# Kernel tuning notes

Hardware: AMD Instinct MI355X
Metric: run time of the kernel (lower is better)

Reference implementation:

```python
import jax, jax.numpy as jnp
import numpy as np

D = 256; NH = 8; NL = 4; NP = 4; DH = D // NH; DFFN = 1024; NQ = 900; BS = 4
SPATIAL = ((92, 92), (46, 46), (23, 23), (12, 12))  # (H, W) per level
LEVEL_START = (0, 8464, 10580, 11109)
S = sum(h * w for h, w in SPATIAL)  # 11253


def _ln(x, g, b):
    m = jnp.mean(x, -1, keepdims=True)
    v = jnp.var(x, -1, keepdims=True)
    return (x - m) / jnp.sqrt(v + 1e-5) * g + b


def setup_inputs() -> dict:
    key = jax.random.key(0)
    ks = jax.random.split(key, 24)
    p = lambda k, s: 0.02 * jax.random.normal(k, s, jnp.float32)
    return {
        "tgt": jax.random.normal(ks[0], (NQ, BS, D), jnp.float32),
        "tgt_query_pos": jax.random.normal(ks[1], (NQ, BS, D), jnp.float32),
        "tgt_reference_points": jax.random.uniform(ks[2], (NQ, BS, NL, 2), jnp.float32),
        "memory": jax.random.normal(ks[3], (S, BS, D), jnp.float32),
        "memory_spatial_shapes": jnp.array(SPATIAL, jnp.int32),
        "memory_level_start_index": jnp.array(LEVEL_START, jnp.int32),
        "in_proj_w": p(ks[4], (3 * D, D)), "in_proj_b": p(ks[5], (3 * D,)),
        "out_proj_w": p(ks[6], (D, D)), "out_proj_b": p(ks[7], (D,)),
        "off_w": p(ks[8], (NH * NL * NP * 2, D)), "off_b": p(ks[9], (NH * NL * NP * 2,)),
        "aw_w": p(ks[10], (NH * NL * NP, D)), "aw_b": p(ks[11], (NH * NL * NP,)),
        "vproj_w": p(ks[12], (D, D)), "vproj_b": p(ks[13], (D,)),
        "oproj_w": p(ks[14], (D, D)), "oproj_b": p(ks[15], (D,)),
        "ln1_g": jnp.ones((D,), jnp.float32), "ln1_b": jnp.zeros((D,), jnp.float32),
        "ln2_g": jnp.ones((D,), jnp.float32), "ln2_b": jnp.zeros((D,), jnp.float32),
        "ln3_g": jnp.ones((D,), jnp.float32), "ln3_b": jnp.zeros((D,), jnp.float32),
        "lin1_w": p(ks[16], (DFFN, D)), "lin1_b": p(ks[17], (DFFN,)),
        "lin2_w": p(ks[18], (D, DFFN)), "lin2_b": p(ks[19], (D,)),
    }


def _self_attn(q, k, v, in_w, in_b, out_w, out_b):
    # q, k, v: (nq, bs, d) -- torch nn.MultiheadAttention, eval mode
    wq, wk, wv = jnp.split(in_w, 3, axis=0)
    bq, bk, bv = jnp.split(in_b, 3)
    qp = (q @ wq.T + bq).reshape(NQ, BS, NH, DH)
    kp = (k @ wk.T + bk).reshape(NQ, BS, NH, DH)
    vp = (v @ wv.T + bv).reshape(NQ, BS, NH, DH)
    s = jnp.einsum("qbhd,kbhd->bhqk", qp, kp) / jnp.sqrt(jnp.float32(DH))
    a = jax.nn.softmax(s, axis=-1)
    o = jnp.einsum("bhqk,kbhd->qbhd", a, vp).reshape(NQ, BS, D)
    return o @ out_w.T + out_b


def _msdeform(x, ref, mem, off_w, off_b, aw_w, aw_b, vproj_w, vproj_b, oproj_w, oproj_b):
    # x: (bs, nq, d); ref: (bs, nq, nl, 2) in [0,1]; mem: (bs, S, d)
    value = (mem @ vproj_w.T + vproj_b).reshape(BS, S, NH, DH)
    off = (x @ off_w.T + off_b).reshape(BS, NQ, NH, NL, NP, 2)
    aw = jax.nn.softmax((x @ aw_w.T + aw_b).reshape(BS, NQ, NH, NL * NP), axis=-1)
    aw = aw.reshape(BS, NQ, NH, NL, NP)
    # offset normalizer = (W, H) per level
    norm = jnp.array([[w, h] for (h, w) in SPATIAL], jnp.float32)
    loc = ref[:, :, None, :, None, :] + off / norm[None, None, None, :, None, :]
    out = jnp.zeros((BS, NH, NQ, DH), x.dtype)
    for l, (H, W) in enumerate(SPATIAL):
        s0 = LEVEL_START[l]
        v = value[:, s0:s0 + H * W].transpose(0, 2, 1, 3)  # (bs, nh, H*W, dh)
        g = loc[:, :, :, l].transpose(0, 2, 1, 3, 4)       # (bs, nh, nq, np, 2)
        # grid_sample align_corners=False, padding_mode='zeros'
        px = g[..., 0] * W - 0.5
        py = g[..., 1] * H - 0.5
        x0 = jnp.floor(px).astype(jnp.int32)
        y0 = jnp.floor(py).astype(jnp.int32)
        wx = px - x0
        wy = py - y0
        samp = jnp.zeros((BS, NH, NQ, NP, DH), x.dtype)
        for dx, dy, w in ((0, 0, (1 - wx) * (1 - wy)), (1, 0, wx * (1 - wy)),
                          (0, 1, (1 - wx) * wy), (1, 1, wx * wy)):
            xi = x0 + dx
            yi = y0 + dy
            valid = ((xi >= 0) & (xi < W) & (yi >= 0) & (yi < H)).astype(x.dtype)
            idx = (jnp.clip(yi, 0, H - 1) * W + jnp.clip(xi, 0, W - 1)).reshape(BS, NH, NQ * NP)
            gat = jnp.take_along_axis(v, idx[..., None], axis=2).reshape(BS, NH, NQ, NP, DH)
            samp = samp + (w * valid)[..., None] * gat
        a = aw[:, :, :, l].transpose(0, 2, 1, 3)  # (bs, nh, nq, np)
        out = out + (samp * a[..., None]).sum(axis=3)
    out = out.transpose(0, 2, 1, 3).reshape(BS, NQ, D)
    return out @ oproj_w.T + oproj_b


def reference(tgt, tgt_query_pos, tgt_reference_points, memory,
              memory_spatial_shapes, memory_level_start_index,
              in_proj_w, in_proj_b, out_proj_w, out_proj_b,
              off_w, off_b, aw_w, aw_b, vproj_w, vproj_b, oproj_w, oproj_b,
              ln1_g, ln1_b, ln2_g, ln2_b, ln3_g, ln3_b,
              lin1_w, lin1_b, lin2_w, lin2_b):
    # module_seq = ['sa', 'ca', 'ffn']; dropout inactive (eval)
    q = tgt + tgt_query_pos
    tgt2 = _self_attn(q, q, tgt, in_proj_w, in_proj_b, out_proj_w, out_proj_b)
    tgt = _ln(tgt + tgt2, ln2_g, ln2_b)
    x = (tgt + tgt_query_pos).transpose(1, 0, 2)
    ref = tgt_reference_points.transpose(1, 0, 2, 3)
    mem = memory.transpose(1, 0, 2)
    tgt2 = _msdeform(x, ref, mem, off_w, off_b, aw_w, aw_b,
                     vproj_w, vproj_b, oproj_w, oproj_b).transpose(1, 0, 2)
    tgt = _ln(tgt + tgt2, ln1_g, ln1_b)
    ff = jax.nn.relu(tgt @ lin1_w.T + lin1_b) @ lin2_w.T + lin2_b
    return _ln(tgt + ff, ln3_g, ln3_b)
```

## Files before the change

### kernel.cpp

```cpp
#include <hip/hip_runtime.h>
#include <math.h>

#define D_MODEL 256
#define NHEAD   8
#define NLVL    4
#define NPTS    4
#define DHEAD   32
#define DFFN    1024
#define NQ      900
#define BSZ     4
#define NROW    (NQ * BSZ)
#define S_TOT   11253
#define VROWS   (S_TOT * BSZ)
#define SASCALE 0.17677669529663687f

typedef __attribute__((ext_vector_type(8))) short short8;
typedef __attribute__((ext_vector_type(4))) float f32x4;
typedef unsigned short ushort_t;

static __device__ __forceinline__ unsigned f2bf1(float f) {
    unsigned u = __float_as_uint(f);
    return (u + 0x7FFFu + ((u >> 16) & 1u)) >> 16;
}
static __device__ __forceinline__ unsigned pack2bf(float x, float y) {
// ... 17 lines not shown

__global__ __launch_bounds__(256) void cvt_weights(
    const float* __restrict__ w_in, const float* __restrict__ w_vp,
    const float* __restrict__ w_outp, const float* __restrict__ w_off,
    const float* __restrict__ w_aw, const float* __restrict__ w_op,
    const float* __restrict__ w_l1, const float* __restrict__ w_l2,
    ushort_t* __restrict__ dst)
{
    int b = blockIdx.x;
    const float* src;
    int dstoff;
    if (b < 96)       { src = w_in;   dstoff = WB_IN;   }
    else if (b < 128) { src = w_vp;   b -= 96;  dstoff = WB_VP;   }
    else if (b < 160) { src = w_outp; b -= 128; dstoff = WB_OUTP; }
    else if (b < 192) { src = w_off;  b -= 160; dstoff = WB_OFF;  }
    else if (b < 208) { src = w_aw;   b -= 192; dstoff = WB_AW;   }
    else if (b < 240) { src = w_op;   b -= 208; dstoff = WB_OP;   }
    else if (b < 368) { src = w_l1;   b -= 240; dstoff = WB_L1;   }
    else              { src = w_l2;   b -= 368; dstoff = WB_L2;   }
    int i = (b * 256 + threadIdx.x) * 8;
    float4 f0 = *(const float4*)(src + i);
    float4 f1 = *(const float4*)(src + i + 4);
    uint4 u;
    u.x = pack2bf(f0.x, f0.y); u.y = pack2bf(f0.z, f0.w);
    u.z = pack2bf(f1.x, f1.y); u.w = pack2bf(f1.z, f1.w);
    *(uint4*)(dst + dstoff + i) = u;
}

__global__ __launch_bounds__(256) void proj_fused(
    const float* __restrict__ tgt, const float* __restrict__ qpos,
    const ushort_t* __restrict__ in_wb, const float* __restrict__ in_b,
    const float* __restrict__ mem, const ushort_t* __restrict__ vp_wb,
    const float* __restrict__ vp_b,
    ushort_t* __restrict__ qkv16, ushort_t* __restrict__ value16)
{
    __shared__ ushort_t As[64 * GPAD];
    __shared__ ushort_t Ws[128 * GPAD];

    const int t    = threadIdx.x;
    const int bid  = blockIdx.x;
    const int trow = t >> 2;
    const int tk   = (t & 3) << 4;
    const int wv   = t >> 6;
    const int ln   = t & 63;
    const int L    = ln & 15;
    const int quad = ln >> 4;

    if (bid < 684) {
        const int m0 = (bid % 57) * 64;
        const int n0 = (bid / 57) * 64;
        const bool addpos = (n0 < 512);
        const float oscale = (n0 < 256) ? SASCALE : 1.f;

        f32x4 acc[4] = {{0.f,0.f,0.f,0.f},{0.f,0.f,0.f,0.f},
                        {0.f,0.f,0.f,0.f},{0.f,0.f,0.f,0.f}};

        for (int k0 = 0; k0 < 256; k0 += 64) {
            {
                int m = m0 + trow;
                float4 a0, a1, a2, a3;
                if (m < NROW) {
                    const float* ap = tgt + (size_t)m * 256 + k0 + tk;
                    a0 = *(const float4*)(ap + 0);
                    a1 = *(const float4*)(ap + 4);
                    a2 = *(const float4*)(ap + 8);
                    a3 = *(const float4*)(ap + 12);
                    if (addpos) {
                        const float* pp = qpos + (size_t)m * 256 + k0 + tk;
                        float4 p0 = *(const float4*)(pp + 0);
                        float4 p1 = *(const float4*)(pp + 4);
                        float4 p2 = *(const float4*)(pp + 8);
                        float4 p3 = *(const float4*)(pp + 12);
                        a0.x += p0.x; a0.y += p0.y; a0.z += p0.z; a0.w += p0.w;
                        a1.x += p1.x; a1.y += p1.y; a1.z += p1.z; a1.w += p1.w;
                        a2.x += p2.x; a2.y += p2.y; a2.z += p2.z; a2.w += p2.w;
                        a3.x += p3.x; a3.y += p3.y; a3.z += p3.z; a3.w += p3.w;
                    }
                } else {
                    a0 = a1 = a2 = a3 = make_float4(0.f, 0.f, 0.f, 0.f);
                }
                uint4 u0, u1;
                u0.x = pack2bf(a0.x, a0.y); u0.y = pack2bf(a0.z, a0.w);
                u0.z = pack2bf(a1.x, a1.y); u0.w = pack2bf(a1.z, a1.w);
                u1.x = pack2bf(a2.x, a2.y); u1.y = pack2bf(a2.z, a2.w);
                u1.z = pack2bf(a3.x, a3.y); u1.w = pack2bf(a3.z, a3.w);
                *(uint4*)&As[trow * GPAD + tk + 0] = u0;
                *(uint4*)&As[trow * GPAD + tk + 8] = u1;
            }
            {
                int n = n0 + trow;
                const ushort_t* wp = in_wb + (size_t)n * 256 + k0 + tk;
                *(uint4*)&Ws[trow * GPAD + tk + 0] = *(const uint4*)(wp + 0);
                *(uint4*)&Ws[trow * GPAD + tk + 8] = *(const uint4*)(wp + 8);
            }
            __syncthreads();
#pragma unroll
            for (int kh = 0; kh < 2; ++kh) {
                short8 af = *(const short8*)&As[(wv * 16 + L) * GPAD + kh * 32 + quad * 8];
#pragma unroll
                for (int cb = 0; cb < 4; ++cb) {
                    short8 bf = *(const short8*)&Ws[(cb * 16 + L) * GPAD + kh * 32 + quad * 8];
                    acc[cb] = __builtin_amdgcn_mfma_f32_16x16x32_bf16(af, bf, acc[cb], 0, 0, 0);
                }
            }
            __syncthreads();
        }
#pragma unroll
        for (int cb = 0; cb < 4; ++cb) {
            int col = n0 + cb * 16 + L;
            float bv = in_b[col];
#pragma unroll
            for (int i = 0; i < 4; ++i) {
                int m = m0 + wv * 16 + quad * 4 + i;
                if (m < NROW)
                    qkv16[(size_t)m * 768 + col] = (ushort_t)f2bf1((acc[cb][i] + bv) * oscale);
            }
        }
    } else {
        const int vb = bid - 684;
        const int m0 = (vb >> 1) * 64;
        const int nh = (vb & 1) * 128;

        f32x4 acc[8];
#pragma unroll
        for (int i = 0; i < 8; ++i) acc[i] = (f32x4){0.f, 0.f, 0.f, 0.f};

        for (int k0 = 0; k0 < 256; k0 += 64) {
            {
                int m = m0 + trow;
                float4 a0, a1, a2, a3;
                if (m < VROWS) {
                    const float* ap = mem + (size_t)m * 256 + k0 + tk;
                    a0 = *(const float4*)(ap + 0);
                    a1 = *(const float4*)(ap + 4);
                    a2 = *(const float4*)(ap + 8);
                    a3 = *(const float4*)(ap + 12);
                } else {
                    a0 = a1 = a2 = a3 = make_float4(0.f, 0.f, 0.f, 0.f);
                }
                uint4 u0, u1;
                u0.x = pack2bf(a0.x, a0.y); u0.y = pack2bf(a0.z, a0.w);
                u0.z = pack2bf(a1.x, a1.y); u0.w = pack2bf(a1.z, a1.w);
                u1.x = pack2bf(a2.x, a2.y); u1.y = pack2bf(a2.z, a2.w);
                u1.z = pack2bf(a3.x, a3.y); u1.w = pack2bf(a3.z, a3.w);
                *(uint4*)&As[trow * GPAD + tk + 0] = u0;
                *(uint4*)&As[trow * GPAD + tk + 8] = u1;
            }
#pragma unroll
            for (int wb = 0; wb < 2; ++wb) {
                int n = wb * 64 + trow;
                const ushort_t* wp = vp_wb + (size_t)(nh + n) * 256 + k0 + tk;
                *(uint4*)&Ws[n * GPAD + tk + 0] = *(const uint4*)(wp + 0);
                *(uint4*)&Ws[n * GPAD + tk + 8] = *(const uint4*)(wp + 8);
            }
            __syncthreads();
#pragma unroll
            for (int kh = 0; kh < 2; ++kh) {
                short8 af = *(const short8*)&As[(wv * 16 + L) * GPAD + kh * 32 + quad * 8];
#pragma unroll
                for (int cb = 0; cb < 8; ++cb) {
                    short8 bf = *(const short8*)&Ws[(cb * 16 + L) * GPAD + kh * 32 + quad * 8];
                    acc[cb] = __builtin_amdgcn_mfma_f32_16x16x32_bf16(af, bf, acc[cb], 0, 0, 0);
                }
            }
            __syncthreads();
        }

        ushort_t* Cs = Ws;
#pragma unroll
        for (int cb = 0; cb < 8; ++cb) {
            int col = cb * 16 + L;
            float bv = vp_b[nh + col];
#pragma unroll
            for (int i = 0; i < 4; ++i) {
                int r = wv * 16 + quad * 4 + i;
                Cs[r * 136 + col] = (ushort_t)f2bf1(acc[cb][i] + bv);
            }
        }
        __syncthreads();
        {
            int r  = t >> 2;
            int ch = (t & 3) * 32;
            int m  = m0 + r;
            if (m < VROWS) {
                const ushort_t* src = &Cs[r * 136 + ch];
                uint4* dst = (uint4*)(value16 + (size_t)m * 256 + nh + ch);
#pragma unroll
                for (int j = 0; j < 4; ++j)
                    dst[j] = *(const uint4*)(src + j * 8);
            }
        }
    }
}

__global__ __launch_bounds__(256) void sa_flash16(
    const ushort_t* __restrict__ qkv, ushort_t* __restrict__ attn_out)
{
    __shared__ ushort_t Ks[2 * 2080];
    __shared__ ushort_t Vt[2 * 2304];
    __shared__ ushort_t Ps[4 * 1152];

    const int t    = threadIdx.x;
    const int q0   = blockIdx.x * 64;
    const int b    = blockIdx.y & 3;
    const int h    = blockIdx.y >> 2;
    const int wv   = t >> 6;
    const int ln   = t & 63;
    const int L    = ln & 15;
    const int quad = ln >> 4;

    union { uint4 u; short8 s; } qu;
    qu.u = make_uint4(0u, 0u, 0u, 0u);
    {
        int q = q0 + wv * 16 + L;
        if (q < NQ)
            qu.u = *(const uint4*)(qkv + ((size_t)q * 4 + b) * 768 + h * 32 + quad * 8);
    }
    const short8 qf = qu.s;

    float mrun = -1e30f, lrun = 0.f;
    f32x4 oacc[2] = {{0.f,0.f,0.f,0.f},{0.f,0.f,0.f,0.f}};

    const int skey = t >> 2;
    const int sdg  = t & 3;

    int it = 0;
    for (int k0 = 0; k0 < NQ; k0 += 64, it ^= 1) {
        {
            int kg = k0 + skey;
            uint4 ku = make_uint4(0u,0u,0u,0u), vu = make_uint4(0u,0u,0u,0u);
            if (kg < NQ) {
                const ushort_t* base = qkv + ((size_t)kg * 4 + b) * 768 + 256 + h * 32 + sdg * 8;
                ku = *(const uint4*)base;
                vu = *(const uint4*)(base + 256);
            }
            *(uint4*)&Ks[it * 2080 + sdg * 520 + skey * 8] = ku;
            ushort_t* vp = &Vt[it * 2304 + sdg * 8 * 72 + skey];
            vp[0 * 72] = (ushort_t)(vu.x & 0xffffu);
            vp[1 * 72] = (ushort_t)(vu.x >> 16);
            vp[2 * 72] = (ushort_t)(vu.y & 0xffffu);
            vp[3 * 72] = (ushort_t)(vu.y >> 16);
            vp[4 * 72] = (ushort_t)(vu.z & 0xffffu);
            vp[5 * 72] = (ushort_t)(vu.z >> 16);
            vp[6 * 72] = (ushort_t)(vu.w & 0xffffu);
            vp[7 * 72] = (ushort_t)(vu.w >> 16);
        }
        __syncthreads();

        f32x4 sacc[4] = {{0.f,0.f,0.f,0.f},{0.f,0.f,0.f,0.f},
                         {0.f,0.f,0.f,0.f},{0.f,0.f,0.f,0.f}};
#pragma unroll
        for (int cb = 0; cb < 4; ++cb) {
            short8 kf = *(const short8*)&Ks[it * 2080 + quad * 520 + (cb * 16 + L) * 8];
            sacc[cb] = __builtin_amdgcn_mfma_f32_16x16x32_bf16(kf, qf, sacc[cb], 0, 0, 0);
        }
        if (k0 + 64 > NQ) {
#pragma unroll
            for (int cb = 0; cb < 4; ++cb)
#pragma unroll
                for (int i = 0; i < 4; ++i)
                    if (k0 + cb * 16 + quad * 4 + i >= NQ) sacc[cb][i] = -1e30f;
        }

        float ml = -1e30f;
#pragma unroll
        for (int cb = 0; cb < 4; ++cb)
#pragma unroll
            for (int i = 0; i < 4; ++i) ml = fmaxf(ml, sacc[cb][i]);
        ml = fmaxf(ml, __shfl_xor(ml, 16, 64));
        ml = fmaxf(ml, __shfl_xor(ml, 32, 64));
        float mnew  = fmaxf(mrun, ml);
        float alpha = __expf(mrun - mnew);
        float p[16];
        float rs = 0.f;
#pragma unroll
        for (int cb = 0; cb < 4; ++cb)
#pragma unroll
            for (int i = 0; i < 4; ++i) {
                float e = __expf(sacc[cb][i] - mnew);
                p[cb * 4 + i] = e;
                rs += e;
            }
        rs += __shfl_xor(rs, 16, 64);
        rs += __shfl_xor(rs, 32, 64);
        lrun = lrun * alpha + rs;
        mrun = mnew;

        {
            ushort_t* pw = &Ps[wv * 1152 + L * 72];
#pragma unroll
            for (int cb = 0; cb < 4; ++cb) {
                uint2 u;
                u.x = pack2bf(p[cb * 4 + 0], p[cb * 4 + 1]);
                u.y = pack2bf(p[cb * 4 + 2], p[cb * 4 + 3]);
                *(uint2*)&pw[cb * 16 + quad * 4] = u;
            }
        }
#pragma unroll
        for (int i = 0; i < 4; ++i) {
            float ai = __shfl(alpha, quad * 4 + i, 64);
            oacc[0][i] *= ai;
            oacc[1][i] *= ai;
        }
        __syncthreads();

#pragma unroll
        for (int ks = 0; ks < 2; ++ks) {
            short8 pf = *(const short8*)&Ps[wv * 1152 + L * 72 + ks * 32 + quad * 8];
#pragma unroll
            for (int db = 0; db < 2; ++db) {
                short8 vf = *(const short8*)&Vt[it * 2304 + (db * 16 + L) * 72 + ks * 32 + quad * 8];
                oacc[db] = __builtin_amdgcn_mfma_f32_16x16x32_bf16(pf, vf, oacc[db], 0, 0, 0);
            }
        }
    }

#pragma unroll
    for (int i = 0; i < 4; ++i) {
        float lq = __shfl(lrun, quad * 4 + i, 64);
        float li = 1.f / lq;
        int q = q0 + wv * 16 + quad * 4 + i;
        if (q < NQ) {
            ushort_t* op = attn_out + ((size_t)q * 4 + b) * 256 + h * 32 + L;
            op[0]  = (ushort_t)f2bf1(oacc[0][i] * li);
            op[16] = (ushort_t)f2bf1(oacc[1][i] * li);
        }
    }
}

__global__ __launch_bounds__(256) void gemm16_f32(
    const ushort_t* __restrict__ A, const ushort_t* __restrict__ W,
    const float* __restrict__ bias, float* __restrict__ C,
    int M, int N, int K, int ldc)
{
    __shared__ ushort_t As[64 * GPAD];
    __shared__ ushort_t Ws[64 * GPAD];

    const int t  = threadIdx.x;
    const int m0 = blockIdx.x * 64;
    const int n0 = blockIdx.y * 64;
    const int trow = t >> 2;
    const int tk   = (t & 3) << 4;
    const int wv   = t >> 6;
    const int ln   = t & 63;
    const int L    = ln & 15;
    const int quad = ln >> 4;

    f32x4 acc[4] = {{0.f,0.f,0.f,0.f},{0.f,0.f,0.f,0.f},
                    {0.f,0.f,0.f,0.f},{0.f,0.f,0.f,0.f}};

    for (int k0 = 0; k0 < K; k0 += 64) {
        {
            int m = m0 + trow;
            uint4 a0 = make_uint4(0u,0u,0u,0u), a1 = make_uint4(0u,0u,0u,0u);
            if (m < M) {
                const ushort_t* ap = A + (size_t)m * K + k0 + tk;
                a0 = *(const uint4*)ap;
                a1 = *(const uint4*)(ap + 8);
            }
            *(uint4*)&As[trow * GPAD + tk + 0] = a0;
            *(uint4*)&As[trow * GPAD + tk + 8] = a1;
        }
        {
            int n = n0 + trow;
            const ushort_t* wp = W + (size_t)n * K + k0 + tk;
            *(uint4*)&Ws[trow * GPAD + tk + 0] = *(const uint4*)(wp + 0);
            *(uint4*)&Ws[trow * GPAD + tk + 8] = *(const uint4*)(wp + 8);
        }
        __syncthreads();
#pragma unroll
        for (int kh = 0; kh < 2; ++kh) {
            short8 af = *(const short8*)&As[(wv * 16 + L) * GPAD + kh * 32 + quad * 8];
#pragma unroll
            for (int cb = 0; cb < 4; ++cb) {
                short8 bf = *(const short8*)&Ws[(cb * 16 + L) * GPAD + kh * 32 + quad * 8];
                acc[cb] = __builtin_amdgcn_mfma_f32_16x16x32_bf16(af, bf, acc[cb], 0, 0, 0);
            }
        }
        __syncthreads();
    }
#pragma unroll
    for (int cb = 0; cb < 4; ++cb) {
        int col = n0 + cb * 16 + L;
        float bv = bias[col];
#pragma unroll
        for (int i = 0; i < 4; ++i) {
            int m = m0 + wv * 16 + quad * 4 + i;
            if (m < M)
                C[(size_t)m * ldc + col] = acc[cb][i] + bv;
        }
    }
}

__global__ __launch_bounds__(256) void ln_resid16(
    const float* __restrict__ xa, const float* __restrict__ xb,
    const float* __restrict__ gam, const float* __restrict__ bet,
    float* __restrict__ out, const float* __restrict__ pos,
    ushort_t* __restrict__ out2)
{
    const int row = blockIdx.x;
    const int t = threadIdx.x;
    float x = xa[(size_t)row * D_MODEL + t] + xb[(size_t)row * D_MODEL + t];
    float s = x, s2 = x * x;
#pragma unroll
    for (int off = 32; off > 0; off >>= 1) {
        s  += __shfl_down(s, off, 64);
        s2 += __shfl_down(s2, off, 64);
    }
    __shared__ float rs[4], rs2[4];
    __shared__ float mean_s, rstd_s;
    int wid = t >> 6, lane = t & 63;
    if (lane == 0) { rs[wid] = s; rs2[wid] = s2; }
    __syncthreads();
    if (t == 0) {
        float S = rs[0] + rs[1] + rs[2] + rs[3];
        float S2 = rs2[0] + rs2[1] + rs2[2] + rs2[3];
        float mean = S * (1.f / 256.f);
        float var = S2 * (1.f / 256.f) - mean * mean;
        mean_s = mean;
        rstd_s = rsqrtf(var + 1e-5f);
    }
    __syncthreads();
    float y = (x - mean_s) * rstd_s * gam[t] + bet[t];
    out[(size_t)row * D_MODEL + t] = y;
    if (out2) {
        float o2 = y + (pos ? pos[(size_t)row * D_MODEL + t] : 0.f);
        out2[(size_t)row * D_MODEL + t] = (ushort_t)f2bf1(o2);
    }
}

__global__ __launch_bounds__(256) void offaw16(
    const ushort_t* __restrict__ A,
    const ushort_t* __restrict__ off_wb, const float* __restrict__ off_b,
    const ushort_t* __restrict__ aw_wb, const float* __restrict__ aw_b,
    float* __restrict__ off_raw, float* __restrict__ aw_raw)
{
    __shared__ ushort_t As[64 * GPAD];
    __shared__ ushort_t Ws[64 * GPAD];

    const int t  = threadIdx.x;
    const int m0 = blockIdx.x * 64;
    const int by = blockIdx.y;
    const bool isaw = (by >= 4);
    const int n0 = isaw ? (by - 4) * 64 : by * 64;
    const ushort_t* W = isaw ? aw_wb : off_wb;
    const float* bs = isaw ? aw_b : off_b;
    float* C = isaw ? aw_raw : off_raw;
    const int ldc = isaw ? 128 : 256;

    const int trow = t >> 2;
    const int tk   = (t & 3) << 4;
    const int wv   = t >> 6;
    const int ln   = t & 63;
    const int L    = ln & 15;
    const int quad = ln >> 4;

    f32x4 acc[4] = {{0.f,0.f,0.f,0.f},{0.f,0.f,0.f,0.f},
                    {0.f,0.f,0.f,0.f},{0.f,0.f,0.f,0.f}};

    for (int k0 = 0; k0 < 256; k0 += 64) {
        {
            int m = m0 + trow;
            uint4 a0 = make_uint4(0u,0u,0u,0u), a1 = make_uint4(0u,0u,0u,0u);
            if (m < NROW) {
                const ushort_t* ap = A + (size_t)m * 256 + k0 + tk;
                a0 = *(const uint4*)ap;
                a1 = *(const uint4*)(ap + 8);
            }
            *(uint4*)&As[trow * GPAD + tk + 0] = a0;
            *(uint4*)&As[trow * GPAD + tk + 8] = a1;
        }
        {
            int n = n0 + trow;
            const ushort_t* wp = W + (size_t)n * 256 + k0 + tk;
            *(uint4*)&Ws[trow * GPAD + tk + 0] = *(const uint4*)(wp + 0);
            *(uint4*)&Ws[trow * GPAD + tk + 8] = *(const uint4*)(wp + 8);
        }
        __syncthreads();
#pragma unroll
        for (int kh = 0; kh < 2; ++kh) {
            short8 af = *(const short8*)&As[(wv * 16 + L) * GPAD + kh * 32 + quad * 8];
#pragma unroll
            for (int cb = 0; cb < 4; ++cb) {
                short8 bf = *(const short8*)&Ws[(cb * 16 + L) * GPAD + kh * 32 + quad * 8];
                acc[cb] = __builtin_amdgcn_mfma_f32_16x16x32_bf16(af, bf, acc[cb], 0, 0, 0);
            }
        }
        __syncthreads();
    }
#pragma unroll
    for (int cb = 0; cb < 4; ++cb) {
        int col = n0 + cb * 16 + L;
        float bv = bs[col];
#pragma unroll
        for (int i = 0; i < 4; ++i) {
            int m = m0 + wv * 16 + quad * 4 + i;
            if (m < NROW)
                C[(size_t)m * ldc + col] = acc[cb][i] + bv;
        }
    }
}

__global__ __launch_bounds__(256) void gemm16_16(
    const ushort_t* __restrict__ A, const ushort_t* __restrict__ W,
    const float* __restrict__ bias, ushort_t* __restrict__ C,
    int M, int N, int K, int ldc, int relu)
{
    __shared__ ushort_t As[64 * GPAD];
    __shared__ ushort_t Ws[64 * GPAD];

    const int t  = threadIdx.x;
    const int m0 = blockIdx.x * 64;
    const int n0 = blockIdx.y * 64;
    const int trow = t >> 2;
    const int tk   = (t & 3) << 4;
    const int wv   = t >> 6;
    const int ln   = t & 63;
    const int L    = ln & 15;
    const int quad = ln >> 4;

    f32x4 acc[4] = {{0.f,0.f,0.f,0.f},{0.f,0.f,0.f,0.f},
                    {0.f,0.f,0.f,0.f},{0.f,0.f,0.f,0.f}};

    for (int k0 = 0; k0 < K; k0 += 64) {
        {
            int m = m0 + trow;
            uint4 a0 = make_uint4(0u,0u,0u,0u), a1 = make_uint4(0u,0u,0u,0u);
            if (m < M) {
                const ushort_t* ap = A + (size_t)m * K + k0 + tk;
                a0 = *(const uint4*)ap;
                a1 = *(const uint4*)(ap + 8);
            }
            *(uint4*)&As[trow * GPAD + tk + 0] = a0;
            *(uint4*)&As[trow * GPAD + tk + 8] = a1;
        }
        {
            int n = n0 + trow;
            const ushort_t* wp = W + (size_t)n * K + k0 + tk;
            *(uint4*)&Ws[trow * GPAD + tk + 0] = *(const uint4*)(wp + 0);
            *(uint4*)&Ws[trow * GPAD + tk + 8] = *(const uint4*)(wp + 8);
        }
        __syncthreads();
#pragma unroll
        for (int kh = 0; kh < 2; ++kh) {
            short8 af = *(const short8*)&As[(wv * 16 + L) * GPAD + kh * 32 + quad * 8];
#pragma unroll
            for (int cb = 0; cb < 4; ++cb) {
                short8 bf = *(const short8*)&Ws[(cb * 16 + L) * GPAD + kh * 32 + quad * 8];
                acc[cb] = __builtin_amdgcn_mfma_f32_16x16x32_bf16(af, bf, acc[cb], 0, 0, 0);
            }
        }
        __syncthreads();
    }
#pragma unroll
    for (int cb = 0; cb < 4; ++cb) {
        int col = n0 + cb * 16 + L;
        float bv = bias[col];
#pragma unroll
        for (int i = 0; i < 4; ++i) {
            int m = m0 + wv * 16 + quad * 4 + i;
            if (m < M) {
                float o = acc[cb][i] + bv;
                if (relu) o = fmaxf(o, 0.f);
                C[(size_t)m * ldc + col] = (ushort_t)f2bf1(o);
            }
        }
    }
}

__global__ __launch_bounds__(256) void msdeform16(
    const float* __restrict__ off_raw, const float* __restrict__ aw_raw,
    const float* __restrict__ refp, const ushort_t* __restrict__ value,
    ushort_t* __restrict__ out)
{
    const int row = blockIdx.x;
    const int b = row & 3;
    const int t = threadIdx.x;

    __shared__ float aw_s[8][17];
    __shared__ float px_s[8][16];
    __shared__ float py_s[8][16];

    const int Hs[4]  = {92, 46, 23, 12};
    const int Wd[4]  = {92, 46, 23, 12};
    const int S0_[4] = {0, 8464, 10580, 11109};

    if (t < 128) {
        int hh = t >> 4, lp = t & 15, l = lp >> 2;
        float ox = off_raw[(size_t)row * 256 + hh * 32 + lp * 2 + 0];
        float oy = off_raw[(size_t)row * 256 + hh * 32 + lp * 2 + 1];
        float rx = refp[((size_t)row * 4 + l) * 2 + 0];
// ... 37 lines not shown
            for (int dy = 0; dy < 2; ++dy) {
#pragma unroll
                for (int dx = 0; dx < 2; ++dx) {
                    int xi = x0 + dx, yi = y0 + dy;
                    float flag = (xi >= 0 && xi < W && yi >= 0 && yi < H) ? 1.f : 0.f;
                    int xc = xi < 0 ? 0 : (xi >= W ? W - 1 : xi);
                    int yc = yi < 0 ? 0 : (yi >= H ? H - 1 : yi);
                    float wgt = (dx ? wx : 1.f - wx) * (dy ? wy : 1.f - wy);
                    float gv = bf2f(vb[(size_t)(base + yc * W + xc) * 1024]);
                    sv = fmaf(wgt * flag, gv, sv);
                }
            }
            acc = fmaf(aw_s[h][lp], sv, acc);
        }
    }
    out[(size_t)row * 256 + h * 32 + d] = (ushort_t)f2bf1(acc);
}

extern "C" void kernel_launch(void* const* d_in, const int* in_sizes, int n_in,
                              void* d_out, int out_size, void* d_ws, size_t ws_size,
                              hipStream_t stream)
{
    const float* tgt    = (const float*)d_in[0];
    const float* qpos   = (const float*)d_in[1];
    const float* refp   = (const float*)d_in[2];
    const float* mem    = (const float*)d_in[3];
    const float* in_w   = (const float*)d_in[6];
    const float* in_b   = (const float*)d_in[7];
    const float* outp_w = (const float*)d_in[8];
    const float* outp_b = (const float*)d_in[9];
    const float* off_w  = (const float*)d_in[10];
    const float* off_b  = (const float*)d_in[11];
    const float* aw_w   = (const float*)d_in[12];
    const float* aw_b   = (const float*)d_in[13];
    const float* vp_w   = (const float*)d_in[14];
    const float* vp_b   = (const float*)d_in[15];
    const float* op_w   = (const float*)d_in[16];
    const float* op_b   = (const float*)d_in[17];
    const float* ln1g   = (const float*)d_in[18];
    const float* ln1b   = (const float*)d_in[19];
    const float* ln2g   = (const float*)d_in[20];
    const float* ln2b   = (const float*)d_in[21];
    const float* ln3g   = (const float*)d_in[22];
    const float* ln3b   = (const float*)d_in[23];
    const float* l1w    = (const float*)d_in[24];
    const float* l1b    = (const float*)d_in[25];
    const float* l2w    = (const float*)d_in[26];
    const float* l2b    = (const float*)d_in[27];
    float* out = (float*)d_out;
    float* ws  = (float*)d_ws;

    ushort_t* qkv16    = (ushort_t*)ws;
    ushort_t* att16    = (ushort_t*)(ws + 691200);
    float*    tmp      = ws + 921600;
    float*    tgt_a    = ws + 1843200;
    ushort_t* xca16    = (ushort_t*)(ws + 2764800);
    float*    off_raw  = ws + 2995200;
    float*    aw_raw   = ws + 3916800;
    ushort_t* att2_16  = (ushort_t*)(ws + 4377600);
    float*    tgt_b    = ws + 4608000;
    ushort_t* tgtb16   = (ushort_t*)(ws + 5529600);
    ushort_t* value16  = (ushort_t*)(ws + 5760000);
    ushort_t* hidden16 = (ushort_t*)(ws + 11521536);
    ushort_t* wb       = (ushort_t*)(ws + 13364736);

    const ushort_t* in_wb   = wb + WB_IN;
    const ushort_t* vp_wb   = wb + WB_VP;
    const ushort_t* outp_wb = wb + WB_OUTP;
    const ushort_t* off_wb  = wb + WB_OFF;
    const ushort_t* aw_wb   = wb + WB_AW;
    const ushort_t* op_wb   = wb + WB_OP;
    const ushort_t* l1_wb   = wb + WB_L1;
    const ushort_t* l2_wb   = wb + WB_L2;

    dim3 b256(256);

    hipLaunchKernelGGL(cvt_weights, dim3(496), b256, 0, stream,
                       in_w, vp_w, outp_w, off_w, aw_w, op_w, l1w, l2w, wb);
    hipLaunchKernelGGL(proj_fused, dim3(2092), b256, 0, stream,
                       tgt, qpos, in_wb, in_b, mem, vp_wb, vp_b, qkv16, value16);
    hipLaunchKernelGGL(sa_flash16, dim3(15, 32), b256, 0, stream, qkv16, att16);
    hipLaunchKernelGGL(gemm16_f32, dim3(57, 4), b256, 0, stream,
                       att16, outp_wb, outp_b, tmp, NROW, 256, 256, 256);
    hipLaunchKernelGGL(ln_resid16, dim3(3600), b256, 0, stream,
                       tgt, tmp, ln2g, ln2b, tgt_a, qpos, xca16);
    hipLaunchKernelGGL(offaw16, dim3(57, 6), b256, 0, stream,
                       xca16, off_wb, off_b, aw_wb, aw_b, off_raw, aw_raw);
    hipLaunchKernelGGL(msdeform16, dim3(3600), b256, 0, stream,
                       off_raw, aw_raw, refp, value16, att2_16);
    hipLaunchKernelGGL(gemm16_f32, dim3(57, 4), b256, 0, stream,
                       att2_16, op_wb, op_b, tmp, NROW, 256, 256, 256);
    hipLaunchKernelGGL(ln_resid16, dim3(3600), b256, 0, stream,
                       tgt_a, tmp, ln1g, ln1b, tgt_b, (const float*)nullptr, tgtb16);
    hipLaunchKernelGGL(gemm16_16, dim3(57, 16), b256, 0, stream,
                       tgtb16, l1_wb, l1b, hidden16, NROW, 1024, 256, 1024, 1);
    hipLaunchKernelGGL(gemm16_f32, dim3(57, 4), b256, 0, stream,
                       hidden16, l2_wb, l2b, tmp, NROW, 256, 1024, 256);
    hipLaunchKernelGGL(ln_resid16, dim3(3600), b256, 0, stream,
                       tgt_b, tmp, ln3g, ln3b, out, (const float*)nullptr, (ushort_t*)nullptr);
}
```

Baseline: 278.9 us.

## Fuse output GEMMs with residual LayerNorm, widen value-proj tile, prefetch K/V

Three GEMM+residual+LayerNorm pairs are merged into one gemm_ln16 kernel. Each block computes a full 64x256 row tile and reduces mean and variance in registers with shuffles, which removes the fp32 tmp round trip and three launches. The value projection now computes all 256 output columns per block, reusing each converted memory tile across both weight halves. Flash self-attention register-prefetches the next K/V tile. Only 57 blocks now cover each fused GEMM, which cuts parallelism, and the 256-row weight tile in shared memory raises per-block footprint.

```diff
diff --git a/kernel.cpp b/kernel.cpp
--- a/kernel.cpp
+++ b/kernel.cpp
@@ -93,44 +93,45 @@
         const bool addpos = (n0 < 512);
         const float oscale = (n0 < 256) ? SASCALE : 1.f;
 
+        const int  mrow = m0 + trow;
+        const bool mv   = (mrow < NROW);
+        const float* arow = tgt  + (size_t)mrow * 256 + tk;
+        const float* prow = qpos + (size_t)mrow * 256 + tk;
+        const ushort_t* wrow = in_wb + (size_t)(n0 + trow) * 256 + tk;
+
         f32x4 acc[4] = {{0.f,0.f,0.f,0.f},{0.f,0.f,0.f,0.f},
                         {0.f,0.f,0.f,0.f},{0.f,0.f,0.f,0.f}};
 
         for (int k0 = 0; k0 < 256; k0 += 64) {
-            {
-                int m = m0 + trow;
-                float4 a0, a1, a2, a3;
-                if (m < NROW) {
-                    const float* ap = tgt + (size_t)m * 256 + k0 + tk;
-                    a0 = *(const float4*)(ap + 0);
-                    a1 = *(const float4*)(ap + 4);
-                    a2 = *(const float4*)(ap + 8);
-                    a3 = *(const float4*)(ap + 12);
-                    if (addpos) {
-                        const float* pp = qpos + (size_t)m * 256 + k0 + tk;
-                        float4 p0 = *(const float4*)(pp + 0);
-                        float4 p1 = *(const float4*)(pp + 4);
-                        float4 p2 = *(const float4*)(pp + 8);
-                        float4 p3 = *(const float4*)(pp + 12);
-                        a0.x += p0.x; a0.y += p0.y; a0.z += p0.z; a0.w += p0.w;
-                        a1.x += p1.x; a1.y += p1.y; a1.z += p1.z; a1.w += p1.w;
-                        a2.x += p2.x; a2.y += p2.y; a2.z += p2.z; a2.w += p2.w;
-                        a3.x += p3.x; a3.y += p3.y; a3.z += p3.z; a3.w += p3.w;
-                    }
-                } else {
-                    a0 = a1 = a2 = a3 = make_float4(0.f, 0.f, 0.f, 0.f);
+            uint4 u0, u1;
+            if (mv) {
+                const float* ap = arow + k0;
+                float4 a0 = *(const float4*)(ap + 0);
+                float4 a1 = *(const float4*)(ap + 4);
+                float4 a2 = *(const float4*)(ap + 8);
+                float4 a3 = *(const float4*)(ap + 12);
+                if (addpos) {
+                    const float* pp = prow + k0;
+                    float4 p0 = *(const float4*)(pp + 0);
+                    float4 p1 = *(const float4*)(pp + 4);
+                    float4 p2 = *(const float4*)(pp + 8);
+                    float4 p3 = *(const float4*)(pp + 12);
+                    a0.x += p0.x; a0.y += p0.y; a0.z += p0.z; a0.w += p0.w;
+                    a1.x += p1.x; a1.y += p1.y; a1.z += p1.z; a1.w += p1.w;
+                    a2.x += p2.x; a2.y += p2.y; a2.z += p2.z; a2.w += p2.w;
+                    a3.x += p3.x; a3.y += p3.y; a3.z += p3.z; a3.w += p3.w;
                 }
-                uint4 u0, u1;
                 u0.x = pack2bf(a0.x, a0.y); u0.y = pack2bf(a0.z, a0.w);
                 u0.z = pack2bf(a1.x, a1.y); u0.w = pack2bf(a1.z, a1.w);
                 u1.x = pack2bf(a2.x, a2.y); u1.y = pack2bf(a2.z, a2.w);
                 u1.z = pack2bf(a3.x, a3.y); u1.w = pack2bf(a3.z, a3.w);
-                *(uint4*)&As[trow * GPAD + tk + 0] = u0;
-                *(uint4*)&As[trow * GPAD + tk + 8] = u1;
-            }
+            } else {
+                u0 = make_uint4(0u, 0u, 0u, 0u); u1 = u0;
+            }
+            *(uint4*)&As[trow * GPAD + tk + 0] = u0;
+            *(uint4*)&As[trow * GPAD + tk + 8] = u1;
             {
-                int n = n0 + trow;
-                const ushort_t* wp = in_wb + (size_t)n * 256 + k0 + tk;
+                const ushort_t* wp = wrow + k0;
                 *(uint4*)&Ws[trow * GPAD + tk + 0] = *(const uint4*)(wp + 0);
                 *(uint4*)&Ws[trow * GPAD + tk + 8] = *(const uint4*)(wp + 8);
             }
@@ -159,38 +160,37 @@
         }
     } else {
         const int vb = bid - 684;
-        const int m0 = (vb >> 1) * 64;
-        const int nh = (vb & 1) * 128;
-
-        f32x4 acc[8];
-#pragma unroll
-        for (int i = 0; i < 8; ++i) acc[i] = (f32x4){0.f, 0.f, 0.f, 0.f};
+        const int m0 = vb * 64;
+
+        const int  mrow = m0 + trow;
+        const bool mv   = (mrow < VROWS);
+        const float* arow = mem + (size_t)mrow * 256 + tk;
+
+        f32x4 acc[16];
+#pragma unroll
+        for (int i = 0; i < 16; ++i) acc[i] = (f32x4){0.f, 0.f, 0.f, 0.f};
 
         for (int k0 = 0; k0 < 256; k0 += 64) {
-            {
-                int m = m0 + trow;
-                float4 a0, a1, a2, a3;
-                if (m < VROWS) {
-                    const float* ap = mem + (size_t)m * 256 + k0 + tk;
-                    a0 = *(const float4*)(ap + 0);
-                    a1 = *(const float4*)(ap + 4);
-                    a2 = *(const float4*)(ap + 8);
-                    a3 = *(const float4*)(ap + 12);
-                } else {
-                    a0 = a1 = a2 = a3 = make_float4(0.f, 0.f, 0.f, 0.f);
-                }
-                uint4 u0, u1;
+            uint4 u0, u1;
+            if (mv) {
+                const float* ap = arow + k0;
+                float4 a0 = *(const float4*)(ap + 0);
+                float4 a1 = *(const float4*)(ap + 4);
+                float4 a2 = *(const float4*)(ap + 8);
+                float4 a3 = *(const float4*)(ap + 12);
                 u0.x = pack2bf(a0.x, a0.y); u0.y = pack2bf(a0.z, a0.w);
                 u0.z = pack2bf(a1.x, a1.y); u0.w = pack2bf(a1.z, a1.w);
                 u1.x = pack2bf(a2.x, a2.y); u1.y = pack2bf(a2.z, a2.w);
                 u1.z = pack2bf(a3.x, a3.y); u1.w = pack2bf(a3.z, a3.w);
-                *(uint4*)&As[trow * GPAD + tk + 0] = u0;
-                *(uint4*)&As[trow * GPAD + tk + 8] = u1;
-            }
-#pragma unroll
-            for (int wb = 0; wb < 2; ++wb) {
-                int n = wb * 64 + trow;
-                const ushort_t* wp = vp_wb + (size_t)(nh + n) * 256 + k0 + tk;
+            } else {
+                u0 = make_uint4(0u, 0u, 0u, 0u); u1 = u0;
+            }
+            *(uint4*)&As[trow * GPAD + tk + 0] = u0;
+            *(uint4*)&As[trow * GPAD + tk + 8] = u1;
+#pragma unroll
+            for (int wg = 0; wg < 2; ++wg) {
+                int n = wg * 64 + trow;
+                const ushort_t* wp = vp_wb + (size_t)n * 256 + k0 + tk;
                 *(uint4*)&Ws[n * GPAD + tk + 0] = *(const uint4*)(wp + 0);
                 *(uint4*)&Ws[n * GPAD + tk + 8] = *(const uint4*)(wp + 8);
             }
@@ -205,30 +205,52 @@
                 }
             }
             __syncthreads();
+#pragma unroll
+            for (int wg = 0; wg < 2; ++wg) {
+                int n = wg * 64 + trow;
+                const ushort_t* wp = vp_wb + (size_t)(128 + n) * 256 + k0 + tk;
+                *(uint4*)&Ws[n * GPAD + tk + 0] = *(const uint4*)(wp + 0);
+                *(uint4*)&Ws[n * GPAD + tk + 8] = *(const uint4*)(wp + 8);
+            }
+            __syncthreads();
+#pragma unroll
+            for (int kh = 0; kh < 2; ++kh) {
+                short8 af = *(const short8*)&As[(wv * 16 + L) * GPAD + kh * 32 + quad * 8];
+#pragma unroll
+                for (int cb = 0; cb < 8; ++cb) {
+                    short8 bf = *(const short8*)&Ws[(cb * 16 + L) * GPAD + kh * 32 + quad * 8];
+                    acc[8 + cb] = __builtin_amdgcn_mfma_f32_16x16x32_bf16(af, bf, acc[8 + cb], 0, 0, 0);
+                }
+            }
+            __syncthreads();
         }
 
         ushort_t* Cs = Ws;
 #pragma unroll
-        for (int cb = 0; cb < 8; ++cb) {
-            int col = cb * 16 + L;
-            float bv = vp_b[nh + col];
-#pragma unroll
-            for (int i = 0; i < 4; ++i) {
-                int r = wv * 16 + quad * 4 + i;
-                Cs[r * 136 + col] = (ushort_t)f2bf1(acc[cb][i] + bv);
-            }
-        }
-        __syncthreads();
-        {
-            int r  = t >> 2;
-            int ch = (t & 3) * 32;
-            int m  = m0 + r;
-            if (m < VROWS) {
-                const ushort_t* src = &Cs[r * 136 + ch];
-                uint4* dst = (uint4*)(value16 + (size_t)m * 256 + nh + ch);
-#pragma unroll
-                for (int j = 0; j < 4; ++j)
-                    dst[j] = *(const uint4*)(src + j * 8);
+        for (int half = 0; half < 2; ++half) {
+            if (half) __syncthreads();
+#pragma unroll
+            for (int cb = 0; cb < 8; ++cb) {
+                int col = cb * 16 + L;
+                float bv = vp_b[half * 128 + col];
+#pragma unroll
+                for (int i = 0; i < 4; ++i) {
+                    int r = wv * 16 + quad * 4 + i;
+                    Cs[r * 136 + col] = (ushort_t)f2bf1(acc[half * 8 + cb][i] + bv);
+                }
+            }
+            __syncthreads();
+            {
+                int r  = t >> 2;
+                int ch = (t & 3) * 32;
+                int m  = m0 + r;
+                if (m < VROWS) {
+                    const ushort_t* src = &Cs[r * 136 + ch];
+                    uint4* dst = (uint4*)(value16 + (size_t)m * 256 + half * 128 + ch);
+#pragma unroll
+                    for (int j = 0; j < 4; ++j)
+                        dst[j] = *(const uint4*)(src + j * 8);
+                }
             }
         }
     }
@@ -265,17 +287,23 @@
     const int skey = t >> 2;
     const int sdg  = t & 3;
 
+    uint4 ku, vu;
+    auto kv_load = [&](int k0) {
+        int kg = k0 + skey;
+        ku = make_uint4(0u, 0u, 0u, 0u);
+        vu = make_uint4(0u, 0u, 0u, 0u);
+        if (kg < NQ) {
+            const ushort_t* base = qkv + ((size_t)kg * 4 + b) * 768 + 256 + h * 32 + sdg * 8;
+            ku = *(const uint4*)base;
+            vu = *(const uint4*)(base + 256);
+        }
+    };
+
+    kv_load(0);
     int it = 0;
     for (int k0 = 0; k0 < NQ; k0 += 64, it ^= 1) {
+        *(uint4*)&Ks[it * 2080 + sdg * 520 + skey * 8] = ku;
         {
-            int kg = k0 + skey;
-            uint4 ku = make_uint4(0u,0u,0u,0u), vu = make_uint4(0u,0u,0u,0u);
-            if (kg < NQ) {
-                const ushort_t* base = qkv + ((size_t)kg * 4 + b) * 768 + 256 + h * 32 + sdg * 8;
-                ku = *(const uint4*)base;
-                vu = *(const uint4*)(base + 256);
-            }
-            *(uint4*)&Ks[it * 2080 + sdg * 520 + skey * 8] = ku;
             ushort_t* vp = &Vt[it * 2304 + sdg * 8 * 72 + skey];
             vp[0 * 72] = (ushort_t)(vu.x & 0xffffu);
             vp[1 * 72] = (ushort_t)(vu.x >> 16);
@@ -287,6 +315,7 @@
             vp[7 * 72] = (ushort_t)(vu.w >> 16);
         }
         __syncthreads();
+        if (k0 + 64 < NQ) kv_load(k0 + 64);
 
         f32x4 sacc[4] = {{0.f,0.f,0.f,0.f},{0.f,0.f,0.f,0.f},
                          {0.f,0.f,0.f,0.f},{0.f,0.f,0.f,0.f}};
@@ -369,10 +398,192 @@
     }
 }
 
-__global__ __launch_bounds__(256) void gemm16_f32(
+__global__ __launch_bounds__(256) void gemm_ln16(
     const ushort_t* __restrict__ A, const ushort_t* __restrict__ W,
-    const float* __restrict__ bias, float* __restrict__ C,
-    int M, int N, int K, int ldc)
+    const float* __restrict__ bias, const float* __restrict__ resid,
+    const float* __restrict__ gam, const float* __restrict__ bet,
+    float* __restrict__ out, const float* __restrict__ pos,
+    ushort_t* __restrict__ out2, int M, int K)
+{
+    __shared__ ushort_t As[64 * GPAD];
+    __shared__ ushort_t Ws[256 * GPAD];
+
+    const int t  = threadIdx.x;
+    const int m0 = blockIdx.x * 64;
+    const int trow = t >> 2;
+    const int tk   = (t & 3) << 4;
+    const int wv   = t >> 6;
+    const int ln   = t & 63;
+    const int L    = ln & 15;
+    const int quad = ln >> 4;
+
+    const int  mrow = m0 + trow;
+    const bool mv   = (mrow < M);
+    const ushort_t* arow = A + (size_t)mrow * K + tk;
+
+    f32x4 acc[16];
+#pragma unroll
+    for (int i = 0; i < 16; ++i) acc[i] = (f32x4){0.f, 0.f, 0.f, 0.f};
+
+    for (int k0 = 0; k0 < K; k0 += 64) {
+        {
+            uint4 a0 = make_uint4(0u,0u,0u,0u), a1 = a0;
+            if (mv) {
+                a0 = *(const uint4*)(arow + k0);
+                a1 = *(const uint4*)(arow + k0 + 8);
+            }
+            *(uint4*)&As[trow * GPAD + tk + 0] = a0;
+            *(uint4*)&As[trow * GPAD + tk + 8] = a1;
+        }
+#pragma unroll
+        for (int wg = 0; wg < 4; ++wg) {
+            int n = wg * 64 + trow;
+            const ushort_t* wp = W + (size_t)n * K + k0 + tk;
+            *(uint4*)&Ws[n * GPAD + tk + 0] = *(const uint4*)(wp + 0);
+            *(uint4*)&Ws[n * GPAD + tk + 8] = *(const uint4*)(wp + 8);
+        }
+        __syncthreads();
+#pragma unroll
+        for (int kh = 0; kh < 2; ++kh) {
+            short8 af = *(const short8*)&As[(wv * 16 + L) * GPAD + kh * 32 + quad * 8];
+#pragma unroll
+            for (int cb = 0; cb < 16; ++cb) {
+                short8 bf = *(const short8*)&Ws[(cb * 16 + L) * GPAD + kh * 32 + quad * 8];
+                acc[cb] = __builtin_amdgcn_mfma_f32_16x16x32_bf16(af, bf, acc[cb], 0, 0, 0);
+            }
+        }
+        __syncthreads();
+    }
+
+    float s[4]  = {0.f, 0.f, 0.f, 0.f};
+    float s2[4] = {0.f, 0.f, 0.f, 0.f};
+#pragma unroll
+    for (int cb = 0; cb < 16; ++cb) {
+        int col = cb * 16 + L;
+        float bv = bias[col];
+#pragma unroll
+        for (int i = 0; i < 4; ++i) {
+            int m = m0 + wv * 16 + quad * 4 + i;
+            float r = (m < M) ? resid[(size_t)m * 256 + col] : 0.f;
+            float xv = acc[cb][i] + bv + r;
+            acc[cb][i] = xv;
+            s[i]  += xv;
+            s2[i] += xv * xv;
+        }
+    }
+#pragma unroll
+    for (int off = 1; off < 16; off <<= 1) {
+#pragma unroll
+        for (int i = 0; i < 4; ++i) {
+            s[i]  += __shfl_xor(s[i],  off, 64);
+            s2[i] += __shfl_xor(s2[i], off, 64);
+        }
+    }
+    float mean[4], rstd[4];
+#pragma unroll
+    for (int i = 0; i < 4; ++i) {
+        mean[i] = s[i] * (1.f / 256.f);
+        float var = s2[i] * (1.f / 256.f) - mean[i] * mean[i];
+        rstd[i] = rsqrtf(var + 1e-5f);
+    }
+#pragma unroll
+    for (int cb = 0; cb < 16; ++cb) {
+        int col = cb * 16 + L;
+        float gv = gam[col];
+        float bt = bet[col];
+#pragma unroll
+        for (int i = 0; i < 4; ++i) {
+            int m = m0 + wv * 16 + quad * 4 + i;
+            if (m < M) {
+                float y = (acc[cb][i] - mean[i]) * rstd[i] * gv + bt;
+                out[(size_t)m * 256 + col] = y;
+                if (out2) {
+                    float o2 = y + (pos ? pos[(size_t)m * 256 + col] : 0.f);
+                    out2[(size_t)m * 256 + col] = (ushort_t)f2bf1(o2);
+                }
+            }
+        }
+    }
+}
+
+__global__ __launch_bounds__(256) void offaw16(
+    const ushort_t* __restrict__ A,
+    const ushort_t* __restrict__ off_wb, const float* __restrict__ off_b,
+    const ushort_t* __restrict__ aw_wb, const float* __restrict__ aw_b,
+    float* __restrict__ off_raw, float* __restrict__ aw_raw)
+{
+    __shared__ ushort_t As[64 * GPAD];
+    __shared__ ushort_t Ws[64 * GPAD];
+
+    const int t  = threadIdx.x;
+    const int m0 = blockIdx.x * 64;
+    const int by = blockIdx.y;
+    const bool isaw = (by >= 4);
+    const int n0 = isaw ? (by - 4) * 64 : by * 64;
+    const ushort_t* W = isaw ? aw_wb : off_wb;
+    const float* bs = isaw ? aw_b : off_b;
+    float* C = isaw ? aw_raw : off_raw;
+    const int ldc = isaw ? 128 : 256;
+
+    const int trow = t >> 2;
+    const int tk   = (t & 3) << 4;
+    const int wv   = t >> 6;
+    const int ln   = t & 63;
+    const int L    = ln & 15;
+    const int quad = ln >> 4;
+
+    const int  mrow = m0 + trow;
+    const bool mv   = (mrow < NROW);
+    const ushort_t* arow = A + (size_t)mrow * 256 + tk;
+    const ushort_t* wrow = W + (size_t)(n0 + trow) * 256 + tk;
+
+    f32x4 acc[4] = {{0.f,0.f,0.f,0.f},{0.f,0.f,0.f,0.f},
+                    {0.f,0.f,0.f,0.f},{0.f,0.f,0.f,0.f}};
+
+    for (int k0 = 0; k0 < 256; k0 += 64) {
+        {
+            uint4 a0 = make_uint4(0u,0u,0u,0u), a1 = a0;
+            if (mv) {
+                a0 = *(const uint4*)(arow + k0);
+                a1 = *(const uint4*)(arow + k0 + 8);
+            }
+            *(uint4*)&As[trow * GPAD + tk + 0] = a0;
+            *(uint4*)&As[trow * GPAD + tk + 8] = a1;
+        }
+        {
+            const ushort_t* wp = wrow + k0;
+            *(uint4*)&Ws[trow * GPAD + tk + 0] = *(const uint4*)(wp + 0);
+            *(uint4*)&Ws[trow * GPAD + tk + 8] = *(const uint4*)(wp + 8);
+        }
+        __syncthreads();
+#pragma unroll
+        for (int kh = 0; kh < 2; ++kh) {
+            short8 af = *(const short8*)&As[(wv * 16 + L) * GPAD + kh * 32 + quad * 8];
+#pragma unroll
+            for (int cb = 0; cb < 4; ++cb) {
+                short8 bf = *(const short8*)&Ws[(cb * 16 + L) * GPAD + kh * 32 + quad * 8];
+                acc[cb] = __builtin_amdgcn_mfma_f32_16x16x32_bf16(af, bf, acc[cb], 0, 0, 0);
+            }
+        }
+        __syncthreads();
+    }
+#pragma unroll
+    for (int cb = 0; cb < 4; ++cb) {
+        int col = n0 + cb * 16 + L;
+        float bv = bs[col];
+#pragma unroll
+        for (int i = 0; i < 4; ++i) {
+            int m = m0 + wv * 16 + quad * 4 + i;
+            if (m < NROW)
+                C[(size_t)m * ldc + col] = acc[cb][i] + bv;
+        }
+    }
+}
+
+__global__ __launch_bounds__(256) void gemm16_16(
+    const ushort_t* __restrict__ A, const ushort_t* __restrict__ W,
+    const float* __restrict__ bias, ushort_t* __restrict__ C,
+    int M, int N, int K, int ldc, int relu)
 {
     __shared__ ushort_t As[64 * GPAD];
     __shared__ ushort_t Ws[64 * GPAD];
@@ -387,197 +598,26 @@
     const int L    = ln & 15;
     const int quad = ln >> 4;
 
+    const int  mrow = m0 + trow;
+    const bool mv   = (mrow < M);
+    const ushort_t* arow = A + (size_t)mrow * K + tk;
+    const ushort_t* wrow = W + (size_t)(n0 + trow) * K + tk;
+
     f32x4 acc[4] = {{0.f,0.f,0.f,0.f},{0.f,0.f,0.f,0.f},
                     {0.f,0.f,0.f,0.f},{0.f,0.f,0.f,0.f}};
 
     for (int k0 = 0; k0 < K; k0 += 64) {
         {
-            int m = m0 + trow;
-            uint4 a0 = make_uint4(0u,0u,0u,0u), a1 = make_uint4(0u,0u,0u,0u);
-            if (m < M) {
-                const ushort_t* ap = A + (size_t)m * K + k0 + tk;
-                a0 = *(const uint4*)ap;
-                a1 = *(const uint4*)(ap + 8);
+            uint4 a0 = make_uint4(0u,0u,0u,0u), a1 = a0;
+            if (mv) {
+                a0 = *(const uint4*)(arow + k0);
+                a1 = *(const uint4*)(arow + k0 + 8);
             }
             *(uint4*)&As[trow * GPAD + tk + 0] = a0;
             *(uint4*)&As[trow * GPAD + tk + 8] = a1;
         }
         {
-            int n = n0 + trow;
-            const ushort_t* wp = W + (size_t)n * K + k0 + tk;
-            *(uint4*)&Ws[trow * GPAD + tk + 0] = *(const uint4*)(wp + 0);
-            *(uint4*)&Ws[trow * GPAD + tk + 8] = *(const uint4*)(wp + 8);
-        }
-        __syncthreads();
-#pragma unroll
-        for (int kh = 0; kh < 2; ++kh) {
-            short8 af = *(const short8*)&As[(wv * 16 + L) * GPAD + kh * 32 + quad * 8];
-#pragma unroll
-            for (int cb = 0; cb < 4; ++cb) {
-                short8 bf = *(const short8*)&Ws[(cb * 16 + L) * GPAD + kh * 32 + quad * 8];
-                acc[cb] = __builtin_amdgcn_mfma_f32_16x16x32_bf16(af, bf, acc[cb], 0, 0, 0);
-            }
-        }
-        __syncthreads();
-    }
-#pragma unroll
-    for (int cb = 0; cb < 4; ++cb) {
-        int col = n0 + cb * 16 + L;
-        float bv = bias[col];
-#pragma unroll
-        for (int i = 0; i < 4; ++i) {
-            int m = m0 + wv * 16 + quad * 4 + i;
-            if (m < M)
-                C[(size_t)m * ldc + col] = acc[cb][i] + bv;
-        }
-    }
-}
-
-__global__ __launch_bounds__(256) void ln_resid16(
-    const float* __restrict__ xa, const float* __restrict__ xb,
-    const float* __restrict__ gam, const float* __restrict__ bet,
-    float* __restrict__ out, const float* __restrict__ pos,
-    ushort_t* __restrict__ out2)
-{
-    const int row = blockIdx.x;
-    const int t = threadIdx.x;
-    float x = xa[(size_t)row * D_MODEL + t] + xb[(size_t)row * D_MODEL + t];
-    float s = x, s2 = x * x;
-#pragma unroll
-    for (int off = 32; off > 0; off >>= 1) {
-        s  += __shfl_down(s, off, 64);
-        s2 += __shfl_down(s2, off, 64);
-    }
-    __shared__ float rs[4], rs2[4];
-    __shared__ float mean_s, rstd_s;
-    int wid = t >> 6, lane = t & 63;
-    if (lane == 0) { rs[wid] = s; rs2[wid] = s2; }
-    __syncthreads();
-    if (t == 0) {
-        float S = rs[0] + rs[1] + rs[2] + rs[3];
-        float S2 = rs2[0] + rs2[1] + rs2[2] + rs2[3];
-        float mean = S * (1.f / 256.f);
-        float var = S2 * (1.f / 256.f) - mean * mean;
-        mean_s = mean;
-        rstd_s = rsqrtf(var + 1e-5f);
-    }
-    __syncthreads();
-    float y = (x - mean_s) * rstd_s * gam[t] + bet[t];
-    out[(size_t)row * D_MODEL + t] = y;
-    if (out2) {
-        float o2 = y + (pos ? pos[(size_t)row * D_MODEL + t] : 0.f);
-        out2[(size_t)row * D_MODEL + t] = (ushort_t)f2bf1(o2);
-    }
-}
-
-__global__ __launch_bounds__(256) void offaw16(
-    const ushort_t* __restrict__ A,
-    const ushort_t* __restrict__ off_wb, const float* __restrict__ off_b,
-    const ushort_t* __restrict__ aw_wb, const float* __restrict__ aw_b,
-    float* __restrict__ off_raw, float* __restrict__ aw_raw)
-{
-    __shared__ ushort_t As[64 * GPAD];
-    __shared__ ushort_t Ws[64 * GPAD];
-
-    const int t  = threadIdx.x;
-    const int m0 = blockIdx.x * 64;
-    const int by = blockIdx.y;
-    const bool isaw = (by >= 4);
-    const int n0 = isaw ? (by - 4) * 64 : by * 64;
-    const ushort_t* W = isaw ? aw_wb : off_wb;
-    const float* bs = isaw ? aw_b : off_b;
-    float* C = isaw ? aw_raw : off_raw;
-    const int ldc = isaw ? 128 : 256;
-
-    const int trow = t >> 2;
-    const int tk   = (t & 3) << 4;
-    const int wv   = t >> 6;
-    const int ln   = t & 63;
-    const int L    = ln & 15;
-    const int quad = ln >> 4;
-
-    f32x4 acc[4] = {{0.f,0.f,0.f,0.f},{0.f,0.f,0.f,0.f},
-                    {0.f,0.f,0.f,0.f},{0.f,0.f,0.f,0.f}};
-
-    for (int k0 = 0; k0 < 256; k0 += 64) {
-        {
-            int m = m0 + trow;
-            uint4 a0 = make_uint4(0u,0u,0u,0u), a1 = make_uint4(0u,0u,0u,0u);
-            if (m < NROW) {
-                const ushort_t* ap = A + (size_t)m * 256 + k0 + tk;
-                a0 = *(const uint4*)ap;
-                a1 = *(const uint4*)(ap + 8);
-            }
-            *(uint4*)&As[trow * GPAD + tk + 0] = a0;
-            *(uint4*)&As[trow * GPAD + tk + 8] = a1;
-        }
-        {
-            int n = n0 + trow;
-            const ushort_t* wp = W + (size_t)n * 256 + k0 + tk;
-            *(uint4*)&Ws[trow * GPAD + tk + 0] = *(const uint4*)(wp + 0);
-            *(uint4*)&Ws[trow * GPAD + tk + 8] = *(const uint4*)(wp + 8);
-        }
-        __syncthreads();
-#pragma unroll
-        for (int kh = 0; kh < 2; ++kh) {
-            short8 af = *(const short8*)&As[(wv * 16 + L) * GPAD + kh * 32 + quad * 8];
-#pragma unroll
-            for (int cb = 0; cb < 4; ++cb) {
-                short8 bf = *(const short8*)&Ws[(cb * 16 + L) * GPAD + kh * 32 + quad * 8];
-                acc[cb] = __builtin_amdgcn_mfma_f32_16x16x32_bf16(af, bf, acc[cb], 0, 0, 0);
-            }
-        }
-        __syncthreads();
-    }
-#pragma unroll
-    for (int cb = 0; cb < 4; ++cb) {
-        int col = n0 + cb * 16 + L;
-        float bv = bs[col];
-#pragma unroll
-        for (int i = 0; i < 4; ++i) {
-            int m = m0 + wv * 16 + quad * 4 + i;
-            if (m < NROW)
-                C[(size_t)m * ldc + col] = acc[cb][i] + bv;
-        }
-    }
-}
-
-__global__ __launch_bounds__(256) void gemm16_16(
-    const ushort_t* __restrict__ A, const ushort_t* __restrict__ W,
-    const float* __restrict__ bias, ushort_t* __restrict__ C,
-    int M, int N, int K, int ldc, int relu)
-{
-    __shared__ ushort_t As[64 * GPAD];
-    __shared__ ushort_t Ws[64 * GPAD];
-
-    const int t  = threadIdx.x;
-    const int m0 = blockIdx.x * 64;
-    const int n0 = blockIdx.y * 64;
-    const int trow = t >> 2;
-    const int tk   = (t & 3) << 4;
-    const int wv   = t >> 6;
-    const int ln   = t & 63;
-    const int L    = ln & 15;
-    const int quad = ln >> 4;
-
-    f32x4 acc[4] = {{0.f,0.f,0.f,0.f},{0.f,0.f,0.f,0.f},
-                    {0.f,0.f,0.f,0.f},{0.f,0.f,0.f,0.f}};
-
-    for (int k0 = 0; k0 < K; k0 += 64) {
-        {
-            int m = m0 + trow;
-            uint4 a0 = make_uint4(0u,0u,0u,0u), a1 = make_uint4(0u,0u,0u,0u);
-            if (m < M) {
-                const ushort_t* ap = A + (size_t)m * K + k0 + tk;
-                a0 = *(const uint4*)ap;
-                a1 = *(const uint4*)(ap + 8);
-            }
-            *(uint4*)&As[trow * GPAD + tk + 0] = a0;
-            *(uint4*)&As[trow * GPAD + tk + 8] = a1;
-        }
-        {
-            int n = n0 + trow;
-            const ushort_t* wp = W + (size_t)n * K + k0 + tk;
+            const ushort_t* wp = wrow + k0;
             *(uint4*)&Ws[trow * GPAD + tk + 0] = *(const uint4*)(wp + 0);
             *(uint4*)&Ws[trow * GPAD + tk + 8] = *(const uint4*)(wp + 8);
         }
@@ -721,7 +761,6 @@
 
     ushort_t* qkv16    = (ushort_t*)ws;
     ushort_t* att16    = (ushort_t*)(ws + 691200);
-    float*    tmp      = ws + 921600;
     float*    tgt_a    = ws + 1843200;
     ushort_t* xca16    = (ushort_t*)(ws + 2764800);
     float*    off_raw  = ws + 2995200;
@@ -746,25 +785,22 @@
 
     hipLaunchKernelGGL(cvt_weights, dim3(496), b256, 0, stream,
                        in_w, vp_w, outp_w, off_w, aw_w, op_w, l1w, l2w, wb);
-    hipLaunchKernelGGL(proj_fused, dim3(2092), b256, 0, stream,
+    hipLaunchKernelGGL(proj_fused, dim3(1388), b256, 0, stream,
                        tgt, qpos, in_wb, in_b, mem, vp_wb, vp_b, qkv16, value16);
     hipLaunchKernelGGL(sa_flash16, dim3(15, 32), b256, 0, stream, qkv16, att16);
-    hipLaunchKernelGGL(gemm16_f32, dim3(57, 4), b256, 0, stream,
-                       att16, outp_wb, outp_b, tmp, NROW, 256, 256, 256);
-    hipLaunchKernelGGL(ln_resid16, dim3(3600), b256, 0, stream,
-                       tgt, tmp, ln2g, ln2b, tgt_a, qpos, xca16);
+    hipLaunchKernelGGL(gemm_ln16, dim3(57), b256, 0, stream,
+                       att16, outp_wb, outp_b, tgt, ln2g, ln2b,
+                       tgt_a, qpos, xca16, NROW, 256);
     hipLaunchKernelGGL(offaw16, dim3(57, 6), b256, 0, stream,
                        xca16, off_wb, off_b, aw_wb, aw_b, off_raw, aw_raw);
     hipLaunchKernelGGL(msdeform16, dim3(3600), b256, 0, stream,
                        off_raw, aw_raw, refp, value16, att2_16);
-    hipLaunchKernelGGL(gemm16_f32, dim3(57, 4), b256, 0, stream,
-                       att2_16, op_wb, op_b, tmp, NROW, 256, 256, 256);
-    hipLaunchKernelGGL(ln_resid16, dim3(3600), b256, 0, stream,
-                       tgt_a, tmp, ln1g, ln1b, tgt_b, (const float*)nullptr, tgtb16);
+    hipLaunchKernelGGL(gemm_ln16, dim3(57), b256, 0, stream,
+                       att2_16, op_wb, op_b, tgt_a, ln1g, ln1b,
+                       tgt_b, (const float*)nullptr, tgtb16, NROW, 256);
     hipLaunchKernelGGL(gemm16_16, dim3(57, 16), b256, 0, stream,
                        tgtb16, l1_wb, l1b, hidden16, NROW, 1024, 256, 1024, 1);
-    hipLaunchKernelGGL(gemm16_f32, dim3(57, 4), b256, 0, stream,
-                       hidden16, l2_wb, l2b, tmp, NROW, 256, 1024, 256);
-    hipLaunchKernelGGL(ln_resid16, dim3(3600), b256, 0, stream,
-                       tgt_b, tmp, ln3g, ln3b, out, (const float*)nullptr, (ushort_t*)nullptr);
-}
+    hipLaunchKernelGGL(gemm_ln16, dim3(57), b256, 0, stream,
+                       hidden16, l2_wb, l2b, tgt_b, ln3g, ln3b,
+                       out, (const float*)nullptr, (ushort_t*)nullptr, NROW, 1024);
+}
```

Result: slower. 359.6 us (+28.9%).
